# Kernel tuning notes

Hardware: AMD Instinct MI355X
Metric: run time of the kernel (lower is better)

Reference implementation:

```python
import jax, jax.numpy as jnp
import numpy as np

DIMS = 1024
HEAD = 16
HEAD_DIM = DIMS // HEAD
B, S = 1, 2048


def setup_inputs() -> dict:
    key = jax.random.key(0)
    ks = jax.random.split(key, 8)
    init = lambda k, shape: (jax.random.normal(k, shape, dtype=jnp.float32) * 0.02)
    x = jax.random.normal(ks[0], (B, S, DIMS), dtype=jnp.float32)
    mask = jnp.zeros((S, S), dtype=jnp.float32)
    Wq = init(ks[1], (DIMS, DIMS)); bq = jnp.zeros((DIMS,), jnp.float32)
    Wk = init(ks[2], (DIMS, DIMS))  # k projection has no bias
    Wv = init(ks[3], (DIMS, DIMS)); bv = jnp.zeros((DIMS,), jnp.float32)
    Wo = init(ks[4], (DIMS, DIMS)); bo = jnp.zeros((DIMS,), jnp.float32)
    Zfactor = jnp.asarray(1e-05, dtype=jnp.float32)
    inv_freq = 1.0 / (10000.0 ** (jnp.arange(0, HEAD_DIM, 2, dtype=jnp.float32) / HEAD_DIM))
    return {"x": x, "mask": mask, "Wq": Wq, "bq": bq, "Wk": Wk, "Wv": Wv,
            "bv": bv, "Wo": Wo, "bo": bo, "Zfactor": Zfactor, "inv_freq": inv_freq}


def _apply_rotary(u, cos, sin):
    # u: [B,H,S,hd]; cos/sin: [S,hd/2]. Pairs are consecutive (view_as_complex).
    a = u[..., 0::2]
    b = u[..., 1::2]
    ra = a * cos - b * sin
    rb = a * sin + b * cos
    return jnp.stack([ra, rb], axis=-1).reshape(u.shape)


def reference(x, mask, Wq, bq, Wk, Wv, bv, Wo, bo, Zfactor, inv_freq):
    Bx, Sx, D = x.shape
    H, hd = HEAD, D // HEAD
    q = x @ Wq.T + bq
    k = x @ Wk.T          # no bias on k
    v = x @ Wv.T + bv
    # [B,S,D] -> [B,H,S,hd]
    split = lambda u: u.reshape(Bx, Sx, H, hd).transpose(0, 2, 1, 3)
    q, k, v = split(q), split(k), split(v)
    # RoPE frequencies: t outer inv_freq -> [S, hd/2]
    t = jnp.arange(Sx, dtype=jnp.float32)
    freqs = t[:, None] * inv_freq[None, :]
    cos, sin = jnp.cos(freqs), jnp.sin(freqs)
    q = _apply_rotary(q, cos, sin)
    k = _apply_rotary(k, cos, sin)
    scale = hd ** (-0.25)
    qk = jnp.einsum('bhqd,bhkd->bhqk', q * scale, k * scale)
    # custom zscale: pad positions (token id 0 taken as first feature of k) get tiny factor
    token_ids = k[..., 0]  # [B,H,Sk]
    zfactor = jnp.clip(jax.nn.softplus(Zfactor), 1e-05, 0.0001)
    zscale = jnp.where(token_ids == 0.0, zfactor, 1.0)  # [B,H,Sk]
    qk = qk + mask[None, None, :Sx, :Sx] * zscale[:, :, None, :]
    qk = qk * zscale[:, :, None, :]
    w = jax.nn.softmax(qk, axis=-1)
    wv = jnp.einsum('bhqk,bhkd->bhqd', w, v)
    wv = wv.transpose(0, 2, 1, 3).reshape(Bx, Sx, D)
    out = wv @ Wo.T + bo
    return out, qk
```

## Files before the change

### kernel.cpp

```cpp
#include <hip/hip_runtime.h>
#include <hip/hip_bf16.h>

#define SEQ 2048
#define DIM 1024
#define NH  16
#define HD  64
#define SPLIT 4
#define KCOLS (SEQ / SPLIT)
#define KVBLK 128
#define CREF 10.0f

typedef __bf16 bf16_t;
typedef __bf16 bf16x4 __attribute__((ext_vector_type(4)));
typedef __bf16 bf16x8 __attribute__((ext_vector_type(8)));
typedef float  f32x4  __attribute__((ext_vector_type(4)));

#define MFMA16(a,b,c) __builtin_amdgcn_mfma_f32_16x16x32_bf16((a),(b),(c),0,0,0)

__device__ __forceinline__ void gload_lds16(const void* g, void* l) {
    __builtin_amdgcn_global_load_lds(
        (const __attribute__((address_space(1))) unsigned int*)g,
        (__attribute__((address_space(3))) unsigned int*)l, 16, 0, 0);
}

__global__ __launch_bounds__(256) void k_tables(const float* __restrict__ invf,
                                                float* __restrict__ cosT,
                                                float* __restrict__ sinT) {
    int id = blockIdx.x * 256 + threadIdx.x;
    int t = id >> 5, i = id & 31;
    float f = (float)t * invf[i];
    cosT[id] = cosf(f);
    sinT[id] = sinf(f);
}

__global__ void k_zeroflag(int* __restrict__ flag) { flag[0] = 0; }

__global__ __launch_bounds__(256) void k_maskchk(const float* __restrict__ mask,
                                                 int* __restrict__ flag) {
    int id = blockIdx.x * 256 + threadIdx.x;
    f32x4 v = *(const f32x4*)(mask + (size_t)id * 4);
    bool nz = (v[0] != 0.f) | (v[1] != 0.f) | (v[2] != 0.f) | (v[3] != 0.f);
    if (__any(nz) && (threadIdx.x & 63) == 0) atomicOr(flag, 1);
}

__global__ __launch_bounds__(256) void k_cvt_all(const float* __restrict__ x,
                                                 const float* __restrict__ Wq,
                                                 const float* __restrict__ Wk,
                                                 const float* __restrict__ Wv,
                                                 const float* __restrict__ Wo,
                                                 bf16_t* __restrict__ Xb,
                                                 bf16_t* __restrict__ Wqkvb,
                                                 bf16_t* __restrict__ Wob) {
    int id = blockIdx.x * 256 + threadIdx.x;
    const float* src;
    bf16_t* dst;
    int off;
    if (id < 524288)       { src = x;  dst = Xb;              off = id; }
    else if (id < 786432)  { src = Wq; dst = Wqkvb;           off = id - 524288; }
    else if (id < 1048576) { src = Wk; dst = Wqkvb + 1048576; off = id - 786432; }
    else if (id < 1310720) { src = Wv; dst = Wqkvb + 2097152; off = id - 1048576; }
    else                   { src = Wo; dst = Wob;             off = id - 1310720; }
    float4 v = ((const float4*)src)[off];
    bf16x4 o;
    o[0] = (bf16_t)v.x; o[1] = (bf16_t)v.y; o[2] = (bf16_t)v.z; o[3] = (bf16_t)v.w;
    ((bf16x4*)dst)[off] = o;
}

__global__ __launch_bounds__(256) void k_biasqkv(const float* __restrict__ bq,
                                                 const float* __restrict__ bv,
                                                 float* __restrict__ bqkv) {
    int n = blockIdx.x * 256 + threadIdx.x;
    bqkv[n] = (n < 1024) ? bq[n] : ((n < 2048) ? 0.0f : bv[n - 2048]);
}

__global__ __launch_bounds__(256) void gemm128(const bf16_t* __restrict__ A,
                                               const bf16_t* __restrict__ W,
                                               const float* __restrict__ bias,
                                               bf16_t* __restrict__ outBf,
                                               float* __restrict__ outF,
                                               int N, int K) {
    __shared__ __align__(16) bf16_t As[2][128 * 32];
    __shared__ __align__(16) bf16_t Bs[2][128 * 32];
    int tid = threadIdx.x, wid = tid >> 6, lane = tid & 63;
    int lrow = lane >> 4, lcol = lane & 15;
    int wr = wid >> 1, wc = wid & 1;

    int orig = blockIdx.y * gridDim.x + blockIdx.x;
    int cpx = (gridDim.x * gridDim.y) >> 3;
    int swzb = (orig & 7) * cpx + (orig >> 3);
    int m0 = (swzb % gridDim.x) * 128;
    int n0 = (swzb / gridDim.x) * 128;

    int sr = wid * 32 + (lane >> 2);
    int sc = (lane & 3) * 8;
    const bf16_t* Ag = A + (size_t)(m0 + sr) * K + sc;
    const bf16_t* Wg = W + (size_t)(n0 + sr) * K + sc;

    f32x4 acc[4][4] = {};

#define STAGE(buf, k0) do { \
        gload_lds16(Ag + (k0),          &As[buf][wid * 1024]);       \
        gload_lds16(Ag + 16 * K + (k0), &As[buf][wid * 1024 + 512]); \
        gload_lds16(Wg + (k0),          &Bs[buf][wid * 1024]);       \
        gload_lds16(Wg + 16 * K + (k0), &Bs[buf][wid * 1024 + 512]); \
    } while (0)

    STAGE(0, 0);
    __syncthreads();
    int buf = 0;
    for (int k0 = 0; k0 < K; k0 += 32) {
        if (k0 + 32 < K) STAGE(buf ^ 1, k0 + 32);
        bf16x8 af[4], bfr[4];
#pragma unroll
        for (int mi = 0; mi < 4; mi++)
            af[mi] = *(const bf16x8*)&As[buf][(wr * 64 + mi * 16 + lcol) * 32 + lrow * 8];
#pragma unroll
        for (int ni = 0; ni < 4; ni++)
            bfr[ni] = *(const bf16x8*)&Bs[buf][(wc * 64 + ni * 16 + lcol) * 32 + lrow * 8];
#pragma unroll
        for (int mi = 0; mi < 4; mi++)
#pragma unroll
            for (int ni = 0; ni < 4; ni++)
                acc[mi][ni] = MFMA16(af[mi], bfr[ni], acc[mi][ni]);
        __syncthreads();
        buf ^= 1;
    }
#undef STAGE
#pragma unroll
    for (int ni = 0; ni < 4; ni++) {
        int col = n0 + wc * 64 + ni * 16 + lcol;
        float bb = bias ? bias[col] : 0.0f;
#pragma unroll
        for (int mi = 0; mi < 4; mi++)
#pragma unroll
            for (int j = 0; j < 4; j++) {
                int row = m0 + wr * 64 + mi * 16 + lrow * 4 + j;
                float v = acc[mi][ni][j] + bb;
                if (outBf) outBf[(size_t)row * N + col] = (bf16_t)v;
                else       outF [(size_t)row * N + col] = v;
            }
    }
}

__global__ __launch_bounds__(256) void k_rope(const bf16_t* __restrict__ QKV,
                                              const float* __restrict__ cosT,
                                              const float* __restrict__ sinT,
                                              const float* __restrict__ Zf,
                                              bf16_t* __restrict__ Qh,
                                              bf16_t* __restrict__ Kh,
                                              float* __restrict__ zsq) {
    int id = blockIdx.x * 256 + threadIdx.x;
    int s = id >> 9, pp = id & 511;
    int h = pp >> 5, i = pp & 31;
    float c  = cosT[s * 32 + i];
    float sn = sinT[s * 32 + i];
    const float scale = 0.3535533905932738f;
    size_t qb = (size_t)s * 3072 + h * HD + 2 * i;
    size_t kb = qb + 1024;
    size_t ob = ((size_t)h * SEQ + s) * HD + 2 * i;

    float qa = (float)QKV[qb], qbv = (float)QKV[qb + 1];
    Qh[ob]     = (bf16_t)((qa * c - qbv * sn) * scale);
    Qh[ob + 1] = (bf16_t)((qa * sn + qbv * c) * scale);

    float k0a = (float)QKV[(size_t)s * 3072 + 1024 + h * HD];
    float k0b = (float)QKV[(size_t)s * 3072 + 1024 + h * HD + 1];
    float ra0 = k0a * cosT[s * 32] - k0b * sinT[s * 32];
    float z = Zf[0];
    float zfac = fminf(fmaxf(log1pf(__expf(z)), 1e-5f), 1e-4f);
    float zs = (ra0 == 0.0f) ? zfac : 1.0f;

    float ka = (float)QKV[kb], kbv = (float)QKV[kb + 1];
    float ra = ka * c - kbv * sn;
    float rb = ka * sn + kbv * c;
    Kh[ob]     = (bf16_t)(ra * scale * zs);
    Kh[ob + 1] = (bf16_t)(rb * scale * zs);
    if (i == 0) zsq[h * SEQ + s] = zs * zs;
}

__global__ __launch_bounds__(256) void k_transpose(const bf16_t* __restrict__ QKV,
                                                   bf16_t* __restrict__ Vt) {
    __shared__ bf16_t tile[64][66];
    int t = threadIdx.x;
    int c = t & 63, r4 = t >> 6;
    int s0 = blockIdx.x * 64, d0 = blockIdx.y * 64;
#pragma unroll
    for (int i = 0; i < 16; i++) {
        int r = i * 4 + r4;
        tile[r][c] = QKV[(size_t)(s0 + r) * 3072 + 2048 + d0 + c];
    }
    __syncthreads();
#pragma unroll
    for (int i = 0; i < 16; i++) {
        int r = i * 4 + r4;
        Vt[(size_t)(d0 + r) * SEQ + s0 + c] = tile[c][r];
    }
}

__global__ __launch_bounds__(256) void k_attn(const bf16_t* __restrict__ Qh,
                                              const bf16_t* __restrict__ Kh,
                                              const bf16_t* __restrict__ Vt,
                                              const float* __restrict__ mask,
                                              const float* __restrict__ zsq,
                                              const int* __restrict__ mflag,
                                              float* __restrict__ qk_out,
                                              bf16_t* __restrict__ Opart,
                                              float* __restrict__ Lpart) {
    __shared__ __align__(16) char Ks[16384];
    __shared__ __align__(16) char Vs[16384];
    __shared__ __align__(16) char Plds[4][4096];
    int tid = threadIdx.x, wid = tid >> 6, lane = tid & 63;
    int lrow = lane >> 4, lcol = lane & 15;
    int h = blockIdx.y, sp = blockIdx.z;
    int q0 = blockIdx.x * 64 + wid * 16;
    int kbase = sp * KCOLS;
    int mz = mflag[0];

    bf16x8 aq[2];
    {
        const bf16_t* qb = Qh + ((size_t)h * SEQ + q0 + lcol) * HD + lrow * 8;
        aq[0] = *(const bf16x8*)qb;
        aq[1] = *(const bf16x8*)(qb + 32);
    }

    float l = 0.f;
    f32x4 acc[4] = {};
    char* wl = &Plds[wid][0];
    float* qkbase = qk_out + (size_t)h * SEQ * SEQ;
    const float* mrow = mask + (size_t)(q0 + lcol) * SEQ;
    const bf16_t* khead = Kh + (size_t)h * SEQ * HD;
    const bf16_t* vthead = Vt + (size_t)h * HD * SEQ;
    const float*  zrow  = zsq + h * SEQ;
    int swzP = (lcol & 7) << 4;
    int l7 = lcol & 7;


    for (int kc = kbase; kc < kbase + KCOLS; kc += KVBLK) {
#pragma unroll
        for (int i = 0; i < 4; i++) {
            int o  = wid * 4096 + i * 1024 + lane * 16;
            int rk = o >> 7, ck = (o >> 4) & 7;
            int sk = ck ^ (rk & 7);
            gload_lds16(khead + (size_t)(kc + rk) * HD + sk * 8,
                        Ks + wid * 4096 + i * 1024);
            int rv = o >> 8, cv = (o >> 4) & 15;
            int sv = (cv & 8) | ((cv & 7) ^ (rv & 7));
            gload_lds16(vthead + (size_t)rv * SEQ + kc + sv * 8,
                        Vs + wid * 4096 + i * 1024);
        }
        __syncthreads();

        float p[8][4];
#pragma unroll
        for (int ct = 0; ct < 8; ct++) {
            int row = ct * 16 + lcol;
            int a0 = row * 128 + ((lrow ^ l7) << 4);
            bf16x8 k0 = *(const bf16x8*)(Ks + a0);
            bf16x8 k1 = *(const bf16x8*)(Ks + (a0 ^ 64));
            f32x4 cacc = {};
            cacc = MFMA16(k0, aq[0], cacc);
            cacc = MFMA16(k1, aq[1], cacc);
#pragma unroll
            for (int j = 0; j < 4; j++) p[ct][j] = cacc[j];
        }
        if (mz) {
#pragma unroll
            for (int ct = 0; ct < 8; ct++) {
                int k4 = kc + ct * 16 + lrow * 4;
                f32x4 mv = *(const f32x4*)(mrow + k4);
                f32x4 zv = *(const f32x4*)(zrow + k4);
#pragma unroll
                for (int j = 0; j < 4; j++)
                    p[ct][j] = fmaf(mv[j], zv[j], p[ct][j]);
            }
        }
#pragma unroll
        for (int ct = 0; ct < 8; ct++) {
            bf16x4 pk;
#pragma unroll
            for (int j = 0; j < 4; j++) {
                float e = __expf(p[ct][j] - CREF);
                l += e;
                pk[j] = (bf16_t)e;
            }
            int addr = (lcol << 8) + ((ct * 16 + lrow * 4) << 1);
            *(bf16x4*)(wl + (addr ^ swzP)) = pk;
        }
        bf16x8 pa[4];
#pragma unroll
        for (int ks = 0; ks < 4; ks++) {
            int addr = (lcol << 8) + (ks << 6) + (lrow << 4);
            pa[ks] = *(const bf16x8*)(wl + (addr ^ swzP));
        }
        __builtin_amdgcn_s_setprio(1);
#pragma unroll
        for (int ks = 0; ks < 4; ks++) {
            int c = ks * 4 + lrow;
            int cs = (c & 8) | ((c & 7) ^ l7);
#pragma unroll
            for (int ng = 0; ng < 4; ng++) {
                int a = (ng * 16 + lcol) * 256 + (cs << 4);
                bf16x8 bv = *(const bf16x8*)(Vs + a);
                acc[ng] = MFMA16(bv, pa[ks], acc[ng]);
            }
        }
        __builtin_amdgcn_s_setprio(0);
#pragma unroll
        for (int ct = 0; ct < 8; ct++) {
            int k4 = kc + ct * 16 + lrow * 4;
            f32x4 ov;
#pragma unroll
            for (int j = 0; j < 4; j++) ov[j] = p[ct][j];
            *(f32x4*)(qkbase + (size_t)(q0 + lcol) * SEQ + k4) = ov;
        }
        __syncthreads();
    }
#pragma unroll
    for (int ng = 0; ng < 4; ng++) {
        bf16x4 o4;
#pragma unroll
        for (int j = 0; j < 4; j++) o4[j] = (bf16_t)acc[ng][j];
        size_t idx = ((size_t)(h * SEQ + q0 + lcol) * SPLIT + sp) * HD + ng * 16 + lrow * 4;
        *(bf16x4*)(Opart + idx) = o4;
    }
    l += __shfl_xor(l, 16);
    l += __shfl_xor(l, 32);
    if (lane < 16) {
        Lpart[((size_t)h * SEQ + q0 + lane) * SPLIT + sp] = l;
    }
}

__global__ __launch_bounds__(256) void k_combine(const bf16_t* __restrict__ Opart,
                                                 const float* __restrict__ Lpart,
                                                 bf16_t* __restrict__ wv) {
    int gid = blockIdx.x * 256 + threadIdx.x;
    int rowIdx = gid >> 6, d = gid & 63;
    const float* lp = Lpart + (size_t)rowIdx * SPLIT;
    float L = 0.f, O = 0.f;
    const bf16_t* ob = Opart + (size_t)rowIdx * SPLIT * HD + d;
#pragma unroll
    for (int s = 0; s < SPLIT; s++) {
        L += lp[s];
        O += (float)ob[(size_t)s * HD];
    }
    int h = rowIdx >> 11, row = rowIdx & (SEQ - 1);
    wv[(size_t)row * DIM + h * HD + d] = (bf16_t)(O / L);
}

extern "C" void kernel_launch(void* const* d_in, const int* in_sizes, int n_in,
                              void* d_out, int out_size, void* d_ws, size_t ws_size,
                              hipStream_t stream) {
    const float* x    = (const float*)d_in[0];
    const float* mask = (const float*)d_in[1];
    const float* Wq   = (const float*)d_in[2];
    const float* bq   = (const float*)d_in[3];
    const float* Wk   = (const float*)d_in[4];
    const float* Wv   = (const float*)d_in[5];
    const float* bv   = (const float*)d_in[6];
    const float* Wo   = (const float*)d_in[7];
    const float* bo   = (const float*)d_in[8];
    const float* Zf   = (const float*)d_in[9];
    const float* invf = (const float*)d_in[10];

    char* ws = (char*)d_ws;
    size_t off = 0;
    auto alloc = [&](size_t bytes) -> char* {
        char* p = ws + off;
        off += (bytes + 255) & ~(size_t)255;
        return p;
    };
    float*  cosT  = (float*)alloc(65536 * 4);
    float*  sinT  = (float*)alloc(65536 * 4);
    bf16_t* Xb    = (bf16_t*)alloc((size_t)SEQ * DIM * 2);
    bf16_t* Wqkvb = (bf16_t*)alloc((size_t)3 * DIM * DIM * 2);
    bf16_t* Wob   = (bf16_t*)alloc((size_t)DIM * DIM * 2);
    float*  bqkv  = (float*)alloc(3072 * 4);
    bf16_t* QKV   = (bf16_t*)alloc((size_t)SEQ * 3 * DIM * 2);
    bf16_t* Qhp   = (bf16_t*)alloc((size_t)SEQ * DIM * 2);
    bf16_t* Khp   = (bf16_t*)alloc((size_t)SEQ * DIM * 2);
    bf16_t* Vt    = (bf16_t*)alloc((size_t)DIM * SEQ * 2);
    float*  zsq   = (float*)alloc((size_t)NH * SEQ * 4);
    bf16_t* Opart = (bf16_t*)alloc((size_t)NH * SEQ * SPLIT * HD * 2);
    float*  Lpart = (float*)alloc((size_t)NH * SEQ * SPLIT * 4);
    bf16_t* WVb   = (bf16_t*)alloc((size_t)SEQ * DIM * 2);
    int*    mflag = (int*)alloc(256);

    float* outp = (float*)d_out;
    float* qkp  = outp + (size_t)SEQ * DIM;

    k_zeroflag<<<1, 1, 0, stream>>>(mflag);
    k_maskchk<<<(SEQ * SEQ / 4) / 256, 256, 0, stream>>>(mask, mflag);
    k_tables<<<256, 256, 0, stream>>>(invf, cosT, sinT);
    k_cvt_all<<<6144, 256, 0, stream>>>(x, Wq, Wk, Wv, Wo, Xb, Wqkvb, Wob);
    k_biasqkv<<<12, 256, 0, stream>>>(bq, bv, bqkv);

    gemm128<<<dim3(SEQ / 128, 3072 / 128), 256, 0, stream>>>(Xb, Wqkvb, bqkv, QKV, nullptr, 3072, DIM);

    k_rope<<<(SEQ * 512) / 256, 256, 0, stream>>>(QKV, cosT, sinT, Zf, Qhp, Khp, zsq);
    k_transpose<<<dim3(SEQ / 64, NH), 256, 0, stream>>>(QKV, Vt);

    k_attn<<<dim3(SEQ / 64, NH, SPLIT), 256, 0, stream>>>(Qhp, Khp, Vt, mask, zsq, mflag,
                                                          qkp, Opart, Lpart);
    k_combine<<<(NH * SEQ * HD) / 256, 256, 0, stream>>>(Opart, Lpart, WVb);

    gemm128<<<dim3(SEQ / 128, DIM / 128), 256, 0, stream>>>(WVb, Wob, bo, nullptr, outp, DIM, DIM);
}
```

Baseline: 173.5 us.

## Double-buffer K/V tiles in LDS to prefetch the next block

K and V shared-memory tiles become two-slot ping-pong buffers. The first tile is loaded before the loop, and each iteration issues async global-to-LDS loads for the next KV block before computing on the current one. The goal is to hide global load latency behind the QK and PV MFMA work and remove one barrier per iteration. In exchange, LDS use per block rises from 48KB to 80KB, which can lower occupancy, and the loop has only four iterations to amortise the prologue.

```diff
diff --git a/kernel.cpp b/kernel.cpp
--- a/kernel.cpp
+++ b/kernel.cpp
@@ -206,8 +206,8 @@
                                               float* __restrict__ qk_out,
                                               bf16_t* __restrict__ Opart,
                                               float* __restrict__ Lpart) {
-    __shared__ __align__(16) char Ks[16384];
-    __shared__ __align__(16) char Vs[16384];
+    __shared__ __align__(16) char Ks[2][16384];
+    __shared__ __align__(16) char Vs[2][16384];
     __shared__ __align__(16) char Plds[4][4096];
     int tid = threadIdx.x, wid = tid >> 6, lane = tid & 63;
     int lrow = lane >> 4, lcol = lane & 15;
@@ -234,29 +234,40 @@
     int swzP = (lcol & 7) << 4;
     int l7 = lcol & 7;
 
+    int so[4], krk[4], ksk[4], vrv[4], vsv[4];
+#pragma unroll
+    for (int i = 0; i < 4; i++) {
+        int o = wid * 4096 + i * 1024 + lane * 16;
+        so[i] = wid * 4096 + i * 1024;
+        krk[i] = o >> 7;
+        ksk[i] = ((o >> 4) & 7) ^ (krk[i] & 7);
+        vrv[i] = o >> 8;
+        int cv = (o >> 4) & 15;
+        vsv[i] = (cv & 8) | ((cv & 7) ^ (vrv[i] & 7));
+    }
+
+#define STAGEKV(b, kc0) do { \
+        _Pragma("unroll") \
+        for (int i = 0; i < 4; i++) { \
+            gload_lds16(khead + (size_t)((kc0) + krk[i]) * HD + ksk[i] * 8, Ks[b] + so[i]); \
+            gload_lds16(vthead + (size_t)vrv[i] * SEQ + (kc0) + vsv[i] * 8,  Vs[b] + so[i]); \
+        } \
+    } while (0)
+
+    STAGEKV(0, kbase);
+    __syncthreads();
+    int buf = 0;
 
     for (int kc = kbase; kc < kbase + KCOLS; kc += KVBLK) {
-#pragma unroll
-        for (int i = 0; i < 4; i++) {
-            int o  = wid * 4096 + i * 1024 + lane * 16;
-            int rk = o >> 7, ck = (o >> 4) & 7;
-            int sk = ck ^ (rk & 7);
-            gload_lds16(khead + (size_t)(kc + rk) * HD + sk * 8,
-                        Ks + wid * 4096 + i * 1024);
-            int rv = o >> 8, cv = (o >> 4) & 15;
-            int sv = (cv & 8) | ((cv & 7) ^ (rv & 7));
-            gload_lds16(vthead + (size_t)rv * SEQ + kc + sv * 8,
-                        Vs + wid * 4096 + i * 1024);
-        }
-        __syncthreads();
+        if (kc + KVBLK < kbase + KCOLS) STAGEKV(buf ^ 1, kc + KVBLK);
 
         float p[8][4];
 #pragma unroll
         for (int ct = 0; ct < 8; ct++) {
             int row = ct * 16 + lcol;
             int a0 = row * 128 + ((lrow ^ l7) << 4);
-            bf16x8 k0 = *(const bf16x8*)(Ks + a0);
-            bf16x8 k1 = *(const bf16x8*)(Ks + (a0 ^ 64));
+            bf16x8 k0 = *(const bf16x8*)(Ks[buf] + a0);
+            bf16x8 k1 = *(const bf16x8*)(Ks[buf] + (a0 ^ 64));
             f32x4 cacc = {};
             cacc = MFMA16(k0, aq[0], cacc);
             cacc = MFMA16(k1, aq[1], cacc);
@@ -300,7 +311,7 @@
 #pragma unroll
             for (int ng = 0; ng < 4; ng++) {
                 int a = (ng * 16 + lcol) * 256 + (cs << 4);
-                bf16x8 bv = *(const bf16x8*)(Vs + a);
+                bf16x8 bv = *(const bf16x8*)(Vs[buf] + a);
                 acc[ng] = MFMA16(bv, pa[ks], acc[ng]);
             }
         }
@@ -314,7 +325,9 @@
             *(f32x4*)(qkbase + (size_t)(q0 + lcol) * SEQ + k4) = ov;
         }
         __syncthreads();
-    }
+        buf ^= 1;
+    }
+#undef STAGEKV
 #pragma unroll
     for (int ng = 0; ng < 4; ng++) {
         bf16x4 o4;
```

New measurement: 172.4 us. About the same (-0.6%).
